# Optimization experiments

Hardware: AMD Instinct MI355X
Metric: run time of the kernel (lower is better)

## Reference

```python
import jax, jax.numpy as jnp
import numpy as np

BASE = 64
EOS = 0
PAD = BASE + 1      # 65
BOS = BASE + 2      # 66
VOCAB = BASE + 3    # 67 (use_bos=True)
NACT = BASE + 1     # 65
H = 512
MAX_LEN = 20
BATCH = 32768


def setup_inputs() -> dict:
    key = jax.random.key(0)
    ks = jax.random.split(key, 12)
    s = 1.0 / np.sqrt(H)  # torch-like init scale, avoids gate saturation
    emb = jax.random.normal(ks[1], (VOCAB, H), jnp.float32) * s
    emb = emb.at[PAD].set(0.0)  # padding_idx row is zero in nn.Embedding
    return {
        'encoded': jax.random.normal(ks[0], (BATCH, H), jnp.float32),
        'emb': emb,
        'W_ih': jax.random.normal(ks[2], (4 * H, H), jnp.float32) * s,
        'W_hh': jax.random.normal(ks[3], (4 * H, H), jnp.float32) * s,
        'b_ih': jax.random.normal(ks[4], (4 * H,), jnp.float32) * s,
        'b_hh': jax.random.normal(ks[5], (4 * H,), jnp.float32) * s,
        'Wc': jax.random.normal(ks[6], (H, H), jnp.float32) * s,
        'bc': jax.random.normal(ks[7], (H,), jnp.float32) * s,
        'Wh': jax.random.normal(ks[8], (H, H), jnp.float32) * s,
        'bh': jax.random.normal(ks[9], (H,), jnp.float32) * s,
        'Wa': jax.random.normal(ks[10], (NACT, H), jnp.float32) * s,
        'ba': jax.random.normal(ks[11], (NACT,), jnp.float32) * s,
    }


def _decode(encoded, emb, W_ih, W_hh, b_ih, b_hh, Wc, bc, Wh, bh, Wa, ba):
    B = encoded.shape[0]
    # NOTE: original passes (cell, hidden) to nn.LSTM, which reads it as (h0, c0).
    h0 = encoded @ Wc.T + bc  # cell_proj output -> used as h0
    c0 = encoded @ Wh.T + bh  # hidden_proj output -> used as c0
    last0 = jnp.full((B,), BOS, jnp.int32)
    stopped0 = jnp.zeros((B,), bool)

    def step(carry, _):
        h, c, last, stopped = carry
        x = emb[last]                                   # [B, H]
        gates = x @ W_ih.T + b_ih + h @ W_hh.T + b_hh   # [B, 4H]
        i, f, g, o = jnp.split(gates, 4, axis=-1)
        c = jax.nn.sigmoid(f) * c + jax.nn.sigmoid(i) * jnp.tanh(g)
        h = jax.nn.sigmoid(o) * jnp.tanh(c)
        logits = h @ Wa.T + ba                          # [B, NACT]
        logp = jax.nn.log_softmax(logits, axis=-1)
        action = jnp.argmax(logits, axis=-1).astype(jnp.int32)  # eval-mode greedy
        alive = (~stopped).astype(logits.dtype)
        ent = -jnp.sum(jnp.exp(logp) * logp, axis=-1) * alive
        lp = jnp.take_along_axis(logp, action[:, None], axis=-1)[:, 0] * alive
        action = jnp.where(stopped, PAD, action)
        stopped = stopped | (action == EOS)
        return (h, c, action, stopped), (action, lp, ent)

    _, (msg, lps, ents) = jax.lax.scan(step, (h0, c0, last0, stopped0), None, length=MAX_LEN)
    message = msg.T                                   # [B, L]
    log_probs = lps.T                                 # [B, L]
    entropy_steps = ents.T                            # [B, L]
    message_len = jnp.sum(message != PAD, axis=1, keepdims=True)  # [B, 1]
    entropy = jnp.sum(entropy_steps, axis=1, keepdims=True) / message_len.astype(entropy_steps.dtype)
    return entropy, log_probs, message, message_len


def reference(encoded, emb, W_ih, W_hh, b_ih, b_hh, Wc, bc, Wh, bh, Wa, ba):
    return _decode(encoded, emb, W_ih, W_hh, b_ih, b_hh, Wc, bc, Wh, bh, Wa, ba)
```

## Files before the change

### kernel.cpp

```cpp
#include <hip/hip_runtime.h>
#include <cmath>


#define HH      512
#define G4      2048
#define NACTS   65
#define NVOCAB  67
#define MAXLEN  20
#define NB      32768
#define TM      16
#define NTH     512
#define EOS_TOK 0
#define PAD_TOK 65
#define BOS_TOK 66
#define HSTR    516

__global__ void prep_gxa_kernel(const float* __restrict__ emb,
                                const float* __restrict__ W_ih,
                                const float* __restrict__ b_ih,
                                const float* __restrict__ b_hh,
                                float* __restrict__ gxa4) {
  int id = blockIdx.x * blockDim.x + threadIdx.x;
  if (id >= NVOCAB * G4) return;
  int a = id / G4, rem = id - a * G4;
  int t = rem >> 2, gate = rem & 3;
  int c = gate * HH + t;
  const float* e = emb + (size_t)a * HH;
  const float* w = W_ih + (size_t)c * HH;
  float acc = 0.f;
  for (int k = 0; k < HH; ++k) acc = fmaf(e[k], w[k], acc);
  gxa4[id] = acc + b_ih[c] + b_hh[c];
}

__global__ void prep_w4_kernel(const float* __restrict__ src,
                               float* __restrict__ dst, int cols) {
  int id = blockIdx.x * blockDim.x + threadIdx.x;
  if (id >= cols * HH) return;
  int k4 = id / (cols * 4);
  int rem = id - k4 * cols * 4;
  int c = rem >> 2, j = rem & 3;
  dst[id] = src[(size_t)c * HH + k4 * 4 + j];
}

__global__ __launch_bounds__(NTH, 4)
void decode_kernel(const float* __restrict__ encoded,
                   const float* __restrict__ gxa4,
                   const float* __restrict__ whh4,
                   const float* __restrict__ wc4,
                   const float* __restrict__ wh4,
                   const float* __restrict__ bc,
                   const float* __restrict__ bh,
                   const float* __restrict__ Wa,
                   const float* __restrict__ ba,
                   float* __restrict__ out) {
  __shared__ float sh_h[TM][HSTR];
  __shared__ float sh_wa[16][HSTR];
  __shared__ float sh_logits[TM][NACTS + 3];
  __shared__ int   sh_last[TM];
  __shared__ int   sh_stop[TM];
  __shared__ float sh_ent[TM];
  __shared__ int   sh_len[TM];

  const int t = threadIdx.x;
  const int row0 = blockIdx.x * TM;

  #pragma unroll
  for (int i = 0; i < (TM * HH / 4) / NTH; ++i) {
    int f4 = i * NTH + t;
    int idx = f4 * 4;
    int r = idx >> 9;
    int c = idx & (HH - 1);
    *reinterpret_cast<float4*>(&sh_h[r][c]) =
        *reinterpret_cast<const float4*>(encoded + (size_t)(row0 + r) * HH + c);
  }
  if (t < TM) { sh_last[t] = BOS_TOK; sh_stop[t] = 0; sh_ent[t] = 0.f; sh_len[t] = 0; }
  __syncthreads();

  float hacc[TM], cacc[TM];
  #pragma unroll
  for (int r = 0; r < TM; ++r) { hacc[r] = 0.f; cacc[r] = 0.f; }
  for (int k4 = 0; k4 < HH / 4; ++k4) {
    float4 wc = *reinterpret_cast<const float4*>(wc4 + ((size_t)k4 * HH + t) * 4);
    float4 wh = *reinterpret_cast<const float4*>(wh4 + ((size_t)k4 * HH + t) * 4);
    #pragma unroll
    for (int r = 0; r < TM; ++r) {
      float4 e = *reinterpret_cast<const float4*>(&sh_h[r][k4 * 4]);
      hacc[r] = fmaf(e.x, wc.x, fmaf(e.y, wc.y, fmaf(e.z, wc.z, fmaf(e.w, wc.w, hacc[r]))));
      cacc[r] = fmaf(e.x, wh.x, fmaf(e.y, wh.y, fmaf(e.z, wh.z, fmaf(e.w, wh.w, cacc[r]))));
    }
  }
  __syncthreads();
  float cst[TM];
  {
    float bcv = bc[t], bhv = bh[t];
    #pragma unroll
    for (int r = 0; r < TM; ++r) {
      sh_h[r][t] = hacc[r] + bcv;
      cst[r] = cacc[r] + bhv;
    }
  }
  __syncthreads();

  for (int step = 0; step < MAXLEN; ++step) {
    float ai[TM], af[TM], ag[TM], ao[TM];
    #pragma unroll
    for (int r = 0; r < TM; ++r) {
      float4 g = *reinterpret_cast<const float4*>(gxa4 + ((size_t)sh_last[r] * HH + t) * 4);
      ai[r] = g.x; af[r] = g.y; ag[r] = g.z; ao[r] = g.w;
    }
    for (int k4 = 0; k4 < HH / 4; ++k4) {
      const float* wb = whh4 + ((size_t)k4 * G4 + t) * 4;
      float4 wi = *reinterpret_cast<const float4*>(wb);
      float4 wf = *reinterpret_cast<const float4*>(wb + 4 * HH);
      float4 wg = *reinterpret_cast<const float4*>(wb + 8 * HH);
      float4 wo = *reinterpret_cast<const float4*>(wb + 12 * HH);
      #pragma unroll
      for (int r = 0; r < TM; ++r) {
        float4 h4 = *reinterpret_cast<const float4*>(&sh_h[r][k4 * 4]);
        ai[r] = fmaf(h4.x, wi.x, fmaf(h4.y, wi.y, fmaf(h4.z, wi.z, fmaf(h4.w, wi.w, ai[r]))));
        af[r] = fmaf(h4.x, wf.x, fmaf(h4.y, wf.y, fmaf(h4.z, wf.z, fmaf(h4.w, wf.w, af[r]))));
        ag[r] = fmaf(h4.x, wg.x, fmaf(h4.y, wg.y, fmaf(h4.z, wg.z, fmaf(h4.w, wg.w, ag[r]))));
        ao[r] = fmaf(h4.x, wo.x, fmaf(h4.y, wo.y, fmaf(h4.z, wo.z, fmaf(h4.w, wo.w, ao[r]))));
      }
    }
    __syncthreads();

    #pragma unroll
    for (int r = 0; r < TM; ++r) {
      float iv = 1.f / (1.f + expf(-ai[r]));
      float fv = 1.f / (1.f + expf(-af[r]));
      float gv = tanhf(ag[r]);
      float ov = 1.f / (1.f + expf(-ao[r]));
      float cn = fmaf(fv, cst[r], iv * gv);
      cst[r] = cn;
      sh_h[r][t] = ov * tanhf(cn);
    }
    __syncthreads();

    const int r_lg = t >> 5;
    const int a_lg = t & 31;
    for (int ab = 0; ab < 5; ++ab) {
      int a0 = ab * 16;
      int arows = (a0 + 16 <= NACTS) ? 16 : (NACTS - a0);
      int total4 = arows * HH / 4;
      for (int f4 = t; f4 < total4; f4 += NTH) {
        int idx = f4 * 4;
        int rr = idx >> 9;
        int cc = idx & (HH - 1);
        *reinterpret_cast<float4*>(&sh_wa[rr][cc]) =
            *reinterpret_cast<const float4*>(Wa + (size_t)(a0 + rr) * HH + cc);
      }
      __syncthreads();
      if (a_lg < arows) {
        float acc = 0.f;
        for (int k4 = 0; k4 < HH / 4; ++k4) {
          float4 h4 = *reinterpret_cast<const float4*>(&sh_h[r_lg][k4 * 4]);
          float4 w4 = *reinterpret_cast<const float4*>(&sh_wa[a_lg][k4 * 4]);
          acc = fmaf(h4.x, w4.x, fmaf(h4.y, w4.y, fmaf(h4.z, w4.z, fmaf(h4.w, w4.w, acc))));
        }
        sh_logits[r_lg][a0 + a_lg] = acc + ba[a0 + a_lg];
      }
      __syncthreads();
    }

    if (t < TM) {
      const int r = t;
      float m = sh_logits[r][0];
      int am = 0;
      for (int a = 1; a < NACTS; ++a) {
        float v = sh_logits[r][a];
        if (v > m) { m = v; am = a; }
      }
      float s = 0.f;
      for (int a = 0; a < NACTS; ++a) s += expf(sh_logits[r][a] - m);
      float logZ = m + logf(s);
      float pl = 0.f;
      for (int a = 0; a < NACTS; ++a) {
        float l = sh_logits[r][a];
        pl = fmaf(expf(l - logZ), l, pl);
      }
      float ent = logZ - pl;
      int stopped = sh_stop[r];
      float lp   = stopped ? 0.f : (sh_logits[r][am] - logZ);
      float entc = stopped ? 0.f : ent;
      int act = stopped ? PAD_TOK : am;
      int grow = row0 + r;
      out[NB + grow * MAXLEN + step] = lp;
      out[NB + NB * MAXLEN + grow * MAXLEN + step] = (float)act;
      sh_ent[r] += entc;
      if (act != PAD_TOK) sh_len[r] += 1;
      if (act == EOS_TOK) sh_stop[r] = 1;
      sh_last[r] = act;
    }
    __syncthreads();
  }

  if (t < TM) {
    int r = t, grow = row0 + r;
    float lenf = (float)sh_len[r];
    out[grow] = sh_ent[r] / lenf;
    out[NB + 2 * NB * MAXLEN + grow] = lenf;
  }
}

extern "C" void kernel_launch(void* const* d_in, const int* in_sizes, int n_in,
                              void* d_out, int out_size, void* d_ws, size_t ws_size,
                              hipStream_t stream) {
  const float* encoded = (const float*)d_in[0];
  const float* emb     = (const float*)d_in[1];
  const float* W_ih    = (const float*)d_in[2];
  const float* W_hh    = (const float*)d_in[3];
  const float* b_ih    = (const float*)d_in[4];
  const float* b_hh    = (const float*)d_in[5];
  const float* Wc      = (const float*)d_in[6];
  const float* bc      = (const float*)d_in[7];
  const float* Wh      = (const float*)d_in[8];
  const float* bh      = (const float*)d_in[9];
  const float* Wa      = (const float*)d_in[10];
  const float* ba      = (const float*)d_in[11];
  float* out = (float*)d_out;

  float* ws   = (float*)d_ws;
  float* gxa4 = ws;
  float* whh4 = gxa4 + NVOCAB * G4;
  float* wc4  = whh4 + (size_t)HH * G4;
  float* wh4  = wc4 + (size_t)HH * HH;

  prep_gxa_kernel<<<(NVOCAB * G4 + 255) / 256, 256, 0, stream>>>(emb, W_ih, b_ih, b_hh, gxa4);
  prep_w4_kernel<<<(G4 * HH + 255) / 256, 256, 0, stream>>>(W_hh, whh4, G4);
  prep_w4_kernel<<<(HH * HH + 255) / 256, 256, 0, stream>>>(Wc, wc4, HH);
  prep_w4_kernel<<<(HH * HH + 255) / 256, 256, 0, stream>>>(Wh, wh4, HH);

  decode_kernel<<<NB / TM, NTH, 0, stream>>>(encoded, gxa4, whh4, wc4, wh4,
                                             bc, bh, Wa, ba, out);
}
```

Baseline: 24.26 ms.

## Halve decode block size so each thread computes two hidden columns

```diff
diff --git a/kernel.cpp b/kernel.cpp
--- a/kernel.cpp
+++ b/kernel.cpp
@@ -9,7 +9,7 @@
 #define MAXLEN  20
 #define NB      32768
 #define TM      16
-#define NTH     512
+#define NTH     256
 #define EOS_TOK 0
 #define PAD_TOK 65
 #define BOS_TOK 66
@@ -42,7 +42,14 @@
   dst[id] = src[(size_t)c * HH + k4 * 4 + j];
 }
 
-__global__ __launch_bounds__(NTH, 4)
+__global__ void ws_sentinel_kernel(float* out) {
+  out[threadIdx.x] = 123000.f;
+}
+
+#define FMA4(acc, h, wv) \
+  acc = fmaf((h).x, (wv).x, fmaf((h).y, (wv).y, fmaf((h).z, (wv).z, fmaf((h).w, (wv).w, (acc)))))
+
+__global__ __launch_bounds__(NTH, 2)
 void decode_kernel(const float* __restrict__ encoded,
                    const float* __restrict__ gxa4,
                    const float* __restrict__ whh4,
@@ -76,69 +83,97 @@
   if (t < TM) { sh_last[t] = BOS_TOK; sh_stop[t] = 0; sh_ent[t] = 0.f; sh_len[t] = 0; }
   __syncthreads();
 
-  float hacc[TM], cacc[TM];
+  float hacc[2][TM], cacc[2][TM];
   #pragma unroll
-  for (int r = 0; r < TM; ++r) { hacc[r] = 0.f; cacc[r] = 0.f; }
+  for (int j = 0; j < 2; ++j)
+    #pragma unroll
+    for (int r = 0; r < TM; ++r) { hacc[j][r] = 0.f; cacc[j][r] = 0.f; }
+  #pragma unroll 1
   for (int k4 = 0; k4 < HH / 4; ++k4) {
-    float4 wc = *reinterpret_cast<const float4*>(wc4 + ((size_t)k4 * HH + t) * 4);
-    float4 wh = *reinterpret_cast<const float4*>(wh4 + ((size_t)k4 * HH + t) * 4);
+    const float* wcb = wc4 + ((size_t)k4 * HH + t) * 4;
+    const float* whb = wh4 + ((size_t)k4 * HH + t) * 4;
+    float4 wc0 = *reinterpret_cast<const float4*>(wcb);
+    float4 wc1 = *reinterpret_cast<const float4*>(wcb + 1024);
+    float4 wh0 = *reinterpret_cast<const float4*>(whb);
+    float4 wh1 = *reinterpret_cast<const float4*>(whb + 1024);
     #pragma unroll
     for (int r = 0; r < TM; ++r) {
       float4 e = *reinterpret_cast<const float4*>(&sh_h[r][k4 * 4]);
-      hacc[r] = fmaf(e.x, wc.x, fmaf(e.y, wc.y, fmaf(e.z, wc.z, fmaf(e.w, wc.w, hacc[r]))));
-      cacc[r] = fmaf(e.x, wh.x, fmaf(e.y, wh.y, fmaf(e.z, wh.z, fmaf(e.w, wh.w, cacc[r]))));
+      FMA4(hacc[0][r], e, wc0);
+      FMA4(hacc[1][r], e, wc1);
+      FMA4(cacc[0][r], e, wh0);
+      FMA4(cacc[1][r], e, wh1);
     }
   }
   __syncthreads();
-  float cst[TM];
+  float cst[2][TM];
   {
-    float bcv = bc[t], bhv = bh[t];
+    float bc0 = bc[t], bc1 = bc[t + 256];
+    float bh0 = bh[t], bh1 = bh[t + 256];
     #pragma unroll
     for (int r = 0; r < TM; ++r) {
-      sh_h[r][t] = hacc[r] + bcv;
-      cst[r] = cacc[r] + bhv;
+      sh_h[r][t] = hacc[0][r] + bc0;
+      sh_h[r][t + 256] = hacc[1][r] + bc1;
+      cst[0][r] = cacc[0][r] + bh0;
+      cst[1][r] = cacc[1][r] + bh1;
     }
   }
   __syncthreads();
 
   for (int step = 0; step < MAXLEN; ++step) {
-    float ai[TM], af[TM], ag[TM], ao[TM];
+    float ai[2][TM], af[2][TM], ag[2][TM], ao[2][TM];
     #pragma unroll
     for (int r = 0; r < TM; ++r) {
-      float4 g = *reinterpret_cast<const float4*>(gxa4 + ((size_t)sh_last[r] * HH + t) * 4);
-      ai[r] = g.x; af[r] = g.y; ag[r] = g.z; ao[r] = g.w;
-    }
+      const float* g0 = gxa4 + ((size_t)sh_last[r] * HH + t) * 4;
+      float4 ga = *reinterpret_cast<const float4*>(g0);
+      float4 gb = *reinterpret_cast<const float4*>(g0 + 1024);
+      ai[0][r] = ga.x; af[0][r] = ga.y; ag[0][r] = ga.z; ao[0][r] = ga.w;
+      ai[1][r] = gb.x; af[1][r] = gb.y; ag[1][r] = gb.z; ao[1][r] = gb.w;
+    }
+    #pragma unroll 1
     for (int k4 = 0; k4 < HH / 4; ++k4) {
-      const float* wb = whh4 + ((size_t)k4 * G4 + t) * 4;
-      float4 wi = *reinterpret_cast<const float4*>(wb);
-      float4 wf = *reinterpret_cast<const float4*>(wb + 4 * HH);
-      float4 wg = *reinterpret_cast<const float4*>(wb + 8 * HH);
-      float4 wo = *reinterpret_cast<const float4*>(wb + 12 * HH);
+      const float* wb = whh4 + (size_t)k4 * (G4 * 4) + t * 4;
+      float4 wi0 = *reinterpret_cast<const float4*>(wb);
+      float4 wf0 = *reinterpret_cast<const float4*>(wb + 2048);
+      float4 wg0 = *reinterpret_cast<const float4*>(wb + 4096);
+      float4 wo0 = *reinterpret_cast<const float4*>(wb + 6144);
+      float4 wi1 = *reinterpret_cast<const float4*>(wb + 1024);
+      float4 wf1 = *reinterpret_cast<const float4*>(wb + 2048 + 1024);
+      float4 wg1 = *reinterpret_cast<const float4*>(wb + 4096 + 1024);
+      float4 wo1 = *reinterpret_cast<const float4*>(wb + 6144 + 1024);
       #pragma unroll
       for (int r = 0; r < TM; ++r) {
         float4 h4 = *reinterpret_cast<const float4*>(&sh_h[r][k4 * 4]);
-        ai[r] = fmaf(h4.x, wi.x, fmaf(h4.y, wi.y, fmaf(h4.z, wi.z, fmaf(h4.w, wi.w, ai[r]))));
-        af[r] = fmaf(h4.x, wf.x, fmaf(h4.y, wf.y, fmaf(h4.z, wf.z, fmaf(h4.w, wf.w, af[r]))));
-        ag[r] = fmaf(h4.x, wg.x, fmaf(h4.y, wg.y, fmaf(h4.z, wg.z, fmaf(h4.w, wg.w, ag[r]))));
-        ao[r] = fmaf(h4.x, wo.x, fmaf(h4.y, wo.y, fmaf(h4.z, wo.z, fmaf(h4.w, wo.w, ao[r]))));
+        FMA4(ai[0][r], h4, wi0);
+        FMA4(af[0][r], h4, wf0);
+        FMA4(ag[0][r], h4, wg0);
+        FMA4(ao[0][r], h4, wo0);
+        FMA4(ai[1][r], h4, wi1);
+        FMA4(af[1][r], h4, wf1);
+        FMA4(ag[1][r], h4, wg1);
+        FMA4(ao[1][r], h4, wo1);
       }
     }
     __syncthreads();
 
     #pragma unroll
-    for (int r = 0; r < TM; ++r) {
-      float iv = 1.f / (1.f + expf(-ai[r]));
-      float fv = 1.f / (1.f + expf(-af[r]));
-      float gv = tanhf(ag[r]);
-      float ov = 1.f / (1.f + expf(-ao[r]));
-      float cn = fmaf(fv, cst[r], iv * gv);
-      cst[r] = cn;
-      sh_h[r][t] = ov * tanhf(cn);
+    for (int j = 0; j < 2; ++j) {
+      int col = t + j * 256;
+      #pragma unroll
+      for (int r = 0; r < TM; ++r) {
+        float iv = 1.f / (1.f + expf(-ai[j][r]));
+        float fv = 1.f / (1.f + expf(-af[j][r]));
+        float gv = tanhf(ag[j][r]);
+        float ov = 1.f / (1.f + expf(-ao[j][r]));
+        float cn = fmaf(fv, cst[j][r], iv * gv);
+        cst[j][r] = cn;
+        sh_h[r][col] = ov * tanhf(cn);
+      }
     }
     __syncthreads();
 
-    const int r_lg = t >> 5;
-    const int a_lg = t & 31;
+    const int r_lg = t >> 4;
+    const int a_lg = t & 15;
     for (int ab = 0; ab < 5; ++ab) {
       int a0 = ab * 16;
       int arows = (a0 + 16 <= NACTS) ? 16 : (NACTS - a0);
@@ -153,10 +188,11 @@
       __syncthreads();
       if (a_lg < arows) {
         float acc = 0.f;
+        #pragma unroll 1
         for (int k4 = 0; k4 < HH / 4; ++k4) {
           float4 h4 = *reinterpret_cast<const float4*>(&sh_h[r_lg][k4 * 4]);
           float4 w4 = *reinterpret_cast<const float4*>(&sh_wa[a_lg][k4 * 4]);
-          acc = fmaf(h4.x, w4.x, fmaf(h4.y, w4.y, fmaf(h4.z, w4.z, fmaf(h4.w, w4.w, acc))));
+          FMA4(acc, h4, w4);
         }
         sh_logits[r_lg][a0 + a_lg] = acc + ba[a0 + a_lg];
       }
@@ -167,14 +203,17 @@
       const int r = t;
       float m = sh_logits[r][0];
       int am = 0;
+      #pragma unroll 1
       for (int a = 1; a < NACTS; ++a) {
         float v = sh_logits[r][a];
         if (v > m) { m = v; am = a; }
       }
       float s = 0.f;
+      #pragma unroll 1
       for (int a = 0; a < NACTS; ++a) s += expf(sh_logits[r][a] - m);
       float logZ = m + logf(s);
       float pl = 0.f;
+      #pragma unroll 1
       for (int a = 0; a < NACTS; ++a) {
         float l = sh_logits[r][a];
         pl = fmaf(expf(l - logZ), l, pl);
@@ -185,8 +224,8 @@
       float entc = stopped ? 0.f : ent;
       int act = stopped ? PAD_TOK : am;
       int grow = row0 + r;
-      out[NB + grow * MAXLEN + step] = lp;
-      out[NB + NB * MAXLEN + grow * MAXLEN + step] = (float)act;
+      out[NB + (size_t)grow * MAXLEN + step] = lp;
+      out[NB + (size_t)NB * MAXLEN + (size_t)grow * MAXLEN + step] = (float)act;
       sh_ent[r] += entc;
       if (act != PAD_TOK) sh_len[r] += 1;
       if (act == EOS_TOK) sh_stop[r] = 1;
@@ -199,7 +238,7 @@
     int r = t, grow = row0 + r;
     float lenf = (float)sh_len[r];
     out[grow] = sh_ent[r] / lenf;
-    out[NB + 2 * NB * MAXLEN + grow] = lenf;
+    out[NB + 2 * (size_t)NB * MAXLEN + grow] = lenf;
   }
 }
 
@@ -220,6 +259,12 @@
   const float* ba      = (const float*)d_in[11];
   float* out = (float*)d_out;
 
+  size_t need = ((size_t)NVOCAB * G4 + (size_t)G4 * HH + 2 * (size_t)HH * HH) * 4;
+  if (ws_size < need) {
+    ws_sentinel_kernel<<<1, 64, 0, stream>>>(out);
+    return;
+  }
+
   float* ws   = (float*)d_ws;
   float* gxa4 = ws;
   float* whh4 = gxa4 + NVOCAB * G4;
```

After: 21.04 ms. 1.15x faster.

## Interleave W_hh gates per thread, read Wa from global, drop logits smem staging

Applied to the files above, without the earlier changes.

```diff
diff --git a/kernel.cpp b/kernel.cpp
--- a/kernel.cpp
+++ b/kernel.cpp
@@ -5,6 +5,7 @@
 #define HH      512
 #define G4      2048
 #define NACTS   65
+#define NAP     80
 #define NVOCAB  67
 #define MAXLEN  20
 #define NB      32768
@@ -42,19 +43,47 @@
   dst[id] = src[(size_t)c * HH + k4 * 4 + j];
 }
 
+__global__ void prep_whh16_kernel(const float* __restrict__ W_hh,
+                                  float* __restrict__ dst) {
+  int id = blockIdx.x * blockDim.x + threadIdx.x;
+  if (id >= 128 * 512 * 16) return;
+  int k4 = id >> 13;
+  int rem = id & 8191;
+  int c = rem >> 4;
+  int q = rem & 15;
+  int g = q >> 2, e = q & 3;
+  dst[id] = W_hh[((size_t)g * 512 + c) * 512 + k4 * 4 + e];
+}
+
+__global__ void prep_wa4_kernel(const float* __restrict__ Wa,
+                                float* __restrict__ dst) {
+  int id = blockIdx.x * blockDim.x + threadIdx.x;
+  if (id >= (HH / 4) * NAP * 4) return;
+  int k4 = id / (NAP * 4);
+  int rem = id - k4 * NAP * 4;
+  int a = rem >> 2, j = rem & 3;
+  dst[id] = (a < NACTS) ? Wa[(size_t)a * HH + k4 * 4 + j] : 0.f;
+}
+
+__global__ void ws_sentinel_kernel(float* out) {
+  out[threadIdx.x] = 123000.f;
+}
+
+#define FMA4(acc, h, wv) \
+  acc = fmaf((h).x, (wv).x, fmaf((h).y, (wv).y, fmaf((h).z, (wv).z, fmaf((h).w, (wv).w, (acc)))))
+
 __global__ __launch_bounds__(NTH, 4)
 void decode_kernel(const float* __restrict__ encoded,
                    const float* __restrict__ gxa4,
-                   const float* __restrict__ whh4,
+                   const float* __restrict__ whh16,
                    const float* __restrict__ wc4,
                    const float* __restrict__ wh4,
                    const float* __restrict__ bc,
                    const float* __restrict__ bh,
-                   const float* __restrict__ Wa,
+                   const float* __restrict__ wa4,
                    const float* __restrict__ ba,
                    float* __restrict__ out) {
   __shared__ float sh_h[TM][HSTR];
-  __shared__ float sh_wa[16][HSTR];
   __shared__ float sh_logits[TM][NACTS + 3];
   __shared__ int   sh_last[TM];
   __shared__ int   sh_stop[TM];
@@ -79,14 +108,15 @@
   float hacc[TM], cacc[TM];
   #pragma unroll
   for (int r = 0; r < TM; ++r) { hacc[r] = 0.f; cacc[r] = 0.f; }
+  #pragma unroll 1
   for (int k4 = 0; k4 < HH / 4; ++k4) {
     float4 wc = *reinterpret_cast<const float4*>(wc4 + ((size_t)k4 * HH + t) * 4);
     float4 wh = *reinterpret_cast<const float4*>(wh4 + ((size_t)k4 * HH + t) * 4);
     #pragma unroll
     for (int r = 0; r < TM; ++r) {
       float4 e = *reinterpret_cast<const float4*>(&sh_h[r][k4 * 4]);
-      hacc[r] = fmaf(e.x, wc.x, fmaf(e.y, wc.y, fmaf(e.z, wc.z, fmaf(e.w, wc.w, hacc[r]))));
-      cacc[r] = fmaf(e.x, wh.x, fmaf(e.y, wh.y, fmaf(e.z, wh.z, fmaf(e.w, wh.w, cacc[r]))));
+      FMA4(hacc[r], e, wc);
+      FMA4(cacc[r], e, wh);
     }
   }
   __syncthreads();
@@ -108,19 +138,22 @@
       float4 g = *reinterpret_cast<const float4*>(gxa4 + ((size_t)sh_last[r] * HH + t) * 4);
       ai[r] = g.x; af[r] = g.y; ag[r] = g.z; ao[r] = g.w;
     }
-    for (int k4 = 0; k4 < HH / 4; ++k4) {
-      const float* wb = whh4 + ((size_t)k4 * G4 + t) * 4;
-      float4 wi = *reinterpret_cast<const float4*>(wb);
-      float4 wf = *reinterpret_cast<const float4*>(wb + 4 * HH);
-      float4 wg = *reinterpret_cast<const float4*>(wb + 8 * HH);
-      float4 wo = *reinterpret_cast<const float4*>(wb + 12 * HH);
-      #pragma unroll
-      for (int r = 0; r < TM; ++r) {
-        float4 h4 = *reinterpret_cast<const float4*>(&sh_h[r][k4 * 4]);
-        ai[r] = fmaf(h4.x, wi.x, fmaf(h4.y, wi.y, fmaf(h4.z, wi.z, fmaf(h4.w, wi.w, ai[r]))));
-        af[r] = fmaf(h4.x, wf.x, fmaf(h4.y, wf.y, fmaf(h4.z, wf.z, fmaf(h4.w, wf.w, af[r]))));
-        ag[r] = fmaf(h4.x, wg.x, fmaf(h4.y, wg.y, fmaf(h4.z, wg.z, fmaf(h4.w, wg.w, ag[r]))));
-        ao[r] = fmaf(h4.x, wo.x, fmaf(h4.y, wo.y, fmaf(h4.z, wo.z, fmaf(h4.w, wo.w, ao[r]))));
+    {
+      const float4* wp = reinterpret_cast<const float4*>(whh16) + (size_t)t * 4;
+      #pragma unroll 1
+      for (int k4 = 0; k4 < HH / 4; ++k4, wp += 2048) {
+        float4 wi = wp[0];
+        float4 wf = wp[1];
+        float4 wg = wp[2];
+        float4 wo = wp[3];
+        #pragma unroll
+        for (int r = 0; r < TM; ++r) {
+          float4 h4 = *reinterpret_cast<const float4*>(&sh_h[r][k4 * 4]);
+          FMA4(ai[r], h4, wi);
+          FMA4(af[r], h4, wf);
+          FMA4(ag[r], h4, wg);
+          FMA4(ao[r], h4, wo);
+        }
       }
     }
     __syncthreads();
@@ -137,44 +170,42 @@
     }
     __syncthreads();
 
-    const int r_lg = t >> 5;
-    const int a_lg = t & 31;
-    for (int ab = 0; ab < 5; ++ab) {
-      int a0 = ab * 16;
-      int arows = (a0 + 16 <= NACTS) ? 16 : (NACTS - a0);
-      int total4 = arows * HH / 4;
-      for (int f4 = t; f4 < total4; f4 += NTH) {
-        int idx = f4 * 4;
-        int rr = idx >> 9;
-        int cc = idx & (HH - 1);
-        *reinterpret_cast<float4*>(&sh_wa[rr][cc]) =
-            *reinterpret_cast<const float4*>(Wa + (size_t)(a0 + rr) * HH + cc);
-      }
-      __syncthreads();
-      if (a_lg < arows) {
+    {
+      const int grp  = t >> 8;
+      const int r_lg = (t >> 4) & 15;
+      const int a_lg = t & 15;
+      const int abB = grp ? 3 : 0;
+      const int abE = grp ? 5 : 3;
+      #pragma unroll 1
+      for (int ab = abB; ab < abE; ++ab) {
+        int a = ab * 16 + a_lg;
         float acc = 0.f;
+        #pragma unroll 4
         for (int k4 = 0; k4 < HH / 4; ++k4) {
           float4 h4 = *reinterpret_cast<const float4*>(&sh_h[r_lg][k4 * 4]);
-          float4 w4 = *reinterpret_cast<const float4*>(&sh_wa[a_lg][k4 * 4]);
-          acc = fmaf(h4.x, w4.x, fmaf(h4.y, w4.y, fmaf(h4.z, w4.z, fmaf(h4.w, w4.w, acc))));
+          float4 w4 = *reinterpret_cast<const float4*>(wa4 + ((size_t)k4 * NAP + a) * 4);
+          FMA4(acc, h4, w4);
         }
-        sh_logits[r_lg][a0 + a_lg] = acc + ba[a0 + a_lg];
-      }
-      __syncthreads();
-    }
+        if (a < NACTS) sh_logits[r_lg][a] = acc + ba[a];
+      }
+    }
+    __syncthreads();
 
     if (t < TM) {
       const int r = t;
       float m = sh_logits[r][0];
       int am = 0;
+      #pragma unroll 1
       for (int a = 1; a < NACTS; ++a) {
         float v = sh_logits[r][a];
         if (v > m) { m = v; am = a; }
       }
       float s = 0.f;
+      #pragma unroll 1
       for (int a = 0; a < NACTS; ++a) s += expf(sh_logits[r][a] - m);
       float logZ = m + logf(s);
       float pl = 0.f;
+      #pragma unroll 1
       for (int a = 0; a < NACTS; ++a) {
         float l = sh_logits[r][a];
         pl = fmaf(expf(l - logZ), l, pl);
@@ -185,8 +216,8 @@
       float entc = stopped ? 0.f : ent;
       int act = stopped ? PAD_TOK : am;
       int grow = row0 + r;
-      out[NB + grow * MAXLEN + step] = lp;
-      out[NB + NB * MAXLEN + grow * MAXLEN + step] = (float)act;
+      out[NB + (size_t)grow * MAXLEN + step] = lp;
+      out[NB + (size_t)NB * MAXLEN + (size_t)grow * MAXLEN + step] = (float)act;
       sh_ent[r] += entc;
       if (act != PAD_TOK) sh_len[r] += 1;
       if (act == EOS_TOK) sh_stop[r] = 1;
@@ -199,7 +230,7 @@
     int r = t, grow = row0 + r;
     float lenf = (float)sh_len[r];
     out[grow] = sh_ent[r] / lenf;
-    out[NB + 2 * NB * MAXLEN + grow] = lenf;
+    out[NB + 2 * (size_t)NB * MAXLEN + grow] = lenf;
   }
 }
 
@@ -220,17 +251,26 @@
   const float* ba      = (const float*)d_in[11];
   float* out = (float*)d_out;
 
-  float* ws   = (float*)d_ws;
-  float* gxa4 = ws;
-  float* whh4 = gxa4 + NVOCAB * G4;
-  float* wc4  = whh4 + (size_t)HH * G4;
-  float* wh4  = wc4 + (size_t)HH * HH;
+  size_t need = ((size_t)NVOCAB * G4 + (size_t)128 * 512 * 16 + 2 * (size_t)HH * HH
+                 + (size_t)(HH / 4) * NAP * 4) * 4;
+  if (ws_size < need) {
+    ws_sentinel_kernel<<<1, 64, 0, stream>>>(out);
+    return;
+  }
+
+  float* ws    = (float*)d_ws;
+  float* gxa4  = ws;
+  float* whh16 = gxa4 + NVOCAB * G4;
+  float* wc4   = whh16 + (size_t)128 * 512 * 16;
+  float* wh4   = wc4 + (size_t)HH * HH;
+  float* wa4   = wh4 + (size_t)HH * HH;
 
   prep_gxa_kernel<<<(NVOCAB * G4 + 255) / 256, 256, 0, stream>>>(emb, W_ih, b_ih, b_hh, gxa4);
-  prep_w4_kernel<<<(G4 * HH + 255) / 256, 256, 0, stream>>>(W_hh, whh4, G4);
+  prep_whh16_kernel<<<(128 * 512 * 16 + 255) / 256, 256, 0, stream>>>(W_hh, whh16);
   prep_w4_kernel<<<(HH * HH + 255) / 256, 256, 0, stream>>>(Wc, wc4, HH);
   prep_w4_kernel<<<(HH * HH + 255) / 256, 256, 0, stream>>>(Wh, wh4, HH);
-
-  decode_kernel<<<NB / TM, NTH, 0, stream>>>(encoded, gxa4, whh4, wc4, wh4,
-                                             bc, bh, Wa, ba, out);
-}
+  prep_wa4_kernel<<<((HH / 4) * NAP * 4 + 255) / 256, 256, 0, stream>>>(Wa, wa4);
+
+  decode_kernel<<<NB / TM, NTH, 0, stream>>>(encoded, gxa4, whh16, wc4, wh4,
+                                             bc, bh, wa4, ba, out);
+}
```

New measurement: 23.55 ms. -2.9%, faster.
